# Kernel tuning notes

Measured on AMD Instinct MI355X. Metric: run time of the kernel, lower is better.

The kernel has to match this reference:

```python
import jax, jax.numpy as jnp
import numpy as np

D_MODEL = 2048
NUM_HEADS = 16
D_HEAD = D_MODEL // NUM_HEADS
ROPE_THETA = 10000.0
MAX_SEQ_LEN = 2048
NEG_INF = -1e30


def _rope_tables(seq_len):
    pos = jnp.arange(seq_len, dtype=jnp.float32)[:, None]          # [s,1]
    i = jnp.arange(0, D_HEAD, 2, dtype=jnp.float32)                 # [d/2]
    freqs = 1.0 / (ROPE_THETA ** (i / D_HEAD))
    angles = pos * freqs                                            # [s, d/2]
    return jnp.cos(angles), jnp.sin(angles)


def _apply_rope(x, cos, sin):
    # x: [b,h,s,d]; interleaved pairs: x1 = even dims, x2 = odd dims
    x1 = x[..., 0::2]
    x2 = x[..., 1::2]
    r1 = x1 * cos - x2 * sin
    r2 = x1 * sin + x2 * cos
    return jnp.stack([r1, r2], axis=-1).reshape(x.shape)


def setup_inputs() -> dict:
    key = jax.random.key(0)
    ks = jax.random.split(key, 5)
    b, s = 2, 2048
    scale = 1.0 / np.sqrt(D_MODEL)  # ~kaiming fan_in scale
    return {
        "x": jax.random.normal(ks[0], (b, s, D_MODEL), jnp.float32),
        "Wq": jax.random.normal(ks[1], (D_MODEL, D_MODEL), jnp.float32) * scale,
        "bq": jnp.zeros((D_MODEL,), jnp.float32),
        "Wk": jax.random.normal(ks[2], (D_MODEL, D_MODEL), jnp.float32) * scale,
        "bk": jnp.zeros((D_MODEL,), jnp.float32),
        "Wv": jax.random.normal(ks[3], (D_MODEL, D_MODEL), jnp.float32) * scale,
        "bv": jnp.zeros((D_MODEL,), jnp.float32),
        "Wo": jax.random.normal(ks[4], (D_MODEL, D_MODEL), jnp.float32) * scale,
        "bo": jnp.zeros((D_MODEL,), jnp.float32),
    }


def reference(x, Wq, bq, Wk, bk, Wv, bv, Wo, bo):
    b, s, _ = x.shape
    # QKV projections (torch Linear: y = x @ W.T + b)
    q = x @ Wq.T + bq
    k = x @ Wk.T + bk
    v = x @ Wv.T + bv
    # split heads: b s (h d) -> b h s d
    def split(t):
        return t.reshape(b, s, NUM_HEADS, D_HEAD).transpose(0, 2, 1, 3)
    q, k, v = split(q), split(k), split(v)
    # RoPE
    cos, sin = _rope_tables(s)
    q = _apply_rope(q, cos, sin)
    k = _apply_rope(k, cos, sin)
    # scaled dot-product attention with causal mask
    scores = jnp.einsum('bhqd,bhkd->bhqk', q, k) / jnp.sqrt(jnp.float32(D_HEAD))
    causal = jnp.tril(jnp.ones((s, s), dtype=bool))
    scores = jnp.where(causal[None, None], scores, NEG_INF)
    attn = jax.nn.softmax(scores, axis=-1)
    out = jnp.einsum('bhqk,bhkd->bhqd', attn, v)
    # merge heads and output projection
    out = out.transpose(0, 2, 1, 3).reshape(b, s, D_MODEL)
    return out @ Wo.T + bo
```

## Files before the change

kernel.cpp:

```cpp
#include <hip/hip_runtime.h>
#include <math.h>

#define D_MODEL 2048
#define NH 16
#define DH 128
#define SEQ 2048
#define NBH 32

typedef unsigned short u16;
typedef unsigned int u32;
typedef __attribute__((ext_vector_type(8))) short short8;
typedef __attribute__((ext_vector_type(4))) float floatx4;
typedef __attribute__((ext_vector_type(4))) unsigned short ushort4v;

__device__ __forceinline__ u16 f2bf(float f) {
  u32 u = __builtin_bit_cast(u32, f);
  return (u16)((u + 0x8000u) >> 16);
}
__device__ __forceinline__ float bf2f(u16 h) {
  return __builtin_bit_cast(float, (u32)h << 16);
}

__device__ __forceinline__ void async_load16(const u16* g, u16* l) {
  __builtin_amdgcn_global_load_lds(
      (const __attribute__((address_space(1))) void*)g,
      (__attribute__((address_space(3))) void*)l, 16, 0, 0);
}

template <int CTRL>
__device__ __forceinline__ float dpp_mov(float x) {
  return __builtin_bit_cast(
      float, __builtin_amdgcn_update_dpp(0, __builtin_bit_cast(int, x), CTRL,
                                         0xf, 0xf, false));
}
__device__ __forceinline__ float rmax16(float x) {
  x = fmaxf(x, dpp_mov<0x121>(x));
  x = fmaxf(x, dpp_mov<0x122>(x));
  x = fmaxf(x, dpp_mov<0x124>(x));
  x = fmaxf(x, dpp_mov<0x128>(x));
  return x;
}
__device__ __forceinline__ float radd16(float x) {
  x += dpp_mov<0x121>(x);
  x += dpp_mov<0x122>(x);
  x += dpp_mov<0x124>(x);
  x += dpp_mov<0x128>(x);
  return x;
}

__global__ void cvt_kernel(const float* __restrict__ src, u16* __restrict__ dst,
                           int n) {
  const int i = (blockIdx.x * 256 + threadIdx.x) * 8;
  if (i >= n) return;
  const floatx4 a = *(const floatx4*)(src + i);
  const floatx4 b = *(const floatx4*)(src + i + 4);
  short8 h;
  h[0] = (short)f2bf(a[0]); h[1] = (short)f2bf(a[1]);
  h[2] = (short)f2bf(a[2]); h[3] = (short)f2bf(a[3]);
  h[4] = (short)f2bf(b[0]); h[5] = (short)f2bf(b[1]);
  h[6] = (short)f2bf(b[2]); h[7] = (short)f2bf(b[3]);
  *(short8*)(dst + i) = h;
}

__global__ __launch_bounds__(256, 2) void gemm_async(
    const u16* __restrict__ A, const u16* __restrict__ W0,
    const u16* __restrict__ W1, const u16* __restrict__ W2,
    const float* __restrict__ b0, const float* __restrict__ b1,
    const float* __restrict__ b2, void* __restrict__ C0, void* __restrict__ C1,
    void* __restrict__ C2, const int qkv) {
  __shared__ u16 As[128 * 64];
  __shared__ u16 Bs[128 * 64];
  const int tid = threadIdx.x;
  const int wave = tid >> 6, lane = tid & 63;
  const int lr = lane & 15, lg = lane >> 4;
  const int m0 = blockIdx.y * 128;
  const int wm = (wave & 1) * 64, wn = (wave >> 1) * 64;

  int n0, mode;
  const u16* W;
  const float* bias;
  void* C;
  if (qkv) {
    const int which = blockIdx.x >> 4;
    n0 = (blockIdx.x & 15) * 128;
    W = which == 0 ? W0 : which == 1 ? W1 : W2;
    bias = which == 0 ? b0 : which == 1 ? b1 : b2;
    C = which == 0 ? C0 : which == 1 ? C1 : C2;
    mode = which;
  } else {
    n0 = blockIdx.x * 128;
    W = W0; bias = b0; C = C0; mode = 3;
  }

  floatx4 acc[4][4];
#pragma unroll
  for (int i = 0; i < 4; ++i)
#pragma unroll
    for (int j = 0; j < 4; ++j) {
      floatx4 z = {0.f, 0.f, 0.f, 0.f};
      acc[i][j] = z;
    }

  for (int kt = 0; kt < D_MODEL; kt += 64) {
#pragma unroll
    for (int p = 0; p < 4; ++p) {
      const int s = p * 256 + tid;
      const int row = s >> 3, c = s & 7;
      const int g = c ^ (row & 7);
      async_load16(A + (size_t)(m0 + row) * D_MODEL + kt + g * 8,
                   &As[(p * 256 + wave * 64) * 8]);
    }
#pragma unroll
    for (int p = 0; p < 4; ++p) {
      const int s = p * 256 + tid;
      const int row = s >> 3, c = s & 7;
      const int g = c ^ (row & 7);
      async_load16(W + (size_t)(n0 + row) * D_MODEL + kt + g * 8,
                   &Bs[(p * 256 + wave * 64) * 8]);
    }
    __syncthreads();

#pragma unroll
    for (int ks = 0; ks < 2; ++ks) {
      short8 af[4], bfr[4];
      const int ch = (ks * 4 + lg) ^ (lr & 7);
#pragma unroll
      for (int i = 0; i < 4; ++i)
        af[i] = *(const short8*)&As[(wm + 16 * i + lr) * 64 + ch * 8];
#pragma unroll
      for (int j = 0; j < 4; ++j)
        bfr[j] = *(const short8*)&Bs[(wn + 16 * j + lr) * 64 + ch * 8];
#pragma unroll
      for (int i = 0; i < 4; ++i)
#pragma unroll
        for (int j = 0; j < 4; ++j)
          acc[i][j] = __builtin_amdgcn_mfma_f32_16x16x32_bf16(af[i], bfr[j],
                                                              acc[i][j], 0, 0, 0);
    }
    __syncthreads();
  }

  float bj[4];
  int ncol[4];
#pragma unroll
  for (int j = 0; j < 4; ++j) {
    ncol[j] = n0 + wn + 16 * j + lr;
    bj[j] = bias[ncol[j]];
  }

  if (mode == 3) {
    float* Cf = (float*)C;
#pragma unroll
    for (int i = 0; i < 4; ++i)
#pragma unroll
      for (int r = 0; r < 4; ++r) {
        const int m = m0 + wm + 16 * i + lg * 4 + r;
#pragma unroll
        for (int j = 0; j < 4; ++j)
          Cf[(size_t)m * D_MODEL + ncol[j]] = acc[i][j][r] + bj[j];
      }
  } else if (mode == 2) {
    u16* Ch = (u16*)C;
#pragma unroll
    for (int i = 0; i < 4; ++i)
#pragma unroll
      for (int r = 0; r < 4; ++r) {
        const int m = m0 + wm + 16 * i + lg * 4 + r;
        const int b = m >> 11, s = m & (SEQ - 1);
#pragma unroll
        for (int j = 0; j < 4; ++j) {
          const int h = ncol[j] >> 7, d = ncol[j] & (DH - 1);
          Ch[((size_t)((b * NH + h) * DH + d)) * SEQ + s] =
              f2bf(acc[i][j][r] + bj[j]);
        }
      }
  } else {
    u16* Ch = (u16*)C;
#pragma unroll
    for (int i = 0; i < 4; ++i)
#pragma unroll
      for (int r = 0; r < 4; ++r) {
        const int m = m0 + wm + 16 * i + lg * 4 + r;
        const int b = m >> 11, s = m & (SEQ - 1);
#pragma unroll
        for (int j = 0; j < 4; ++j) {
          const int h = ncol[j] >> 7, d = ncol[j] & (DH - 1);
          Ch[((size_t)((b * NH + h) * SEQ + s)) * DH + d] =
              f2bf(acc[i][j][r] + bj[j]);
        }
      }
  }
}

__global__ void rope_kernel(u16* __restrict__ Q, u16* __restrict__ K) {
  const int idx = blockIdx.x * blockDim.x + threadIdx.x;
  const int p = idx & 63;
  const int s = (idx >> 6) & (SEQ - 1);
  const int bh = idx >> 17;
  if (bh >= NBH) return;
  const float freq = exp2f(-(float)p * (13.287712379549449f / 64.0f));
  const float ang = (float)s * freq;
  float sn, cs;
  sincosf(ang, &sn, &cs);
  const size_t base = ((size_t)bh * SEQ + s) * DH + 2 * p;
  {
    const u32 qq = *(const u32*)(Q + base);
    const float x1 = bf2f((u16)(qq & 0xffffu)), x2 = bf2f((u16)(qq >> 16));
    *(u32*)(Q + base) =
        (u32)f2bf(x1 * cs - x2 * sn) | ((u32)f2bf(x1 * sn + x2 * cs) << 16);
  }
  {
    const u32 kk = *(const u32*)(K + base);
    const float x1 = bf2f((u16)(kk & 0xffffu)), x2 = bf2f((u16)(kk >> 16));
    *(u32*)(K + base) =
        (u32)f2bf(x1 * cs - x2 * sn) | ((u32)f2bf(x1 * sn + x2 * cs) << 16);
  }
}

__global__ __launch_bounds__(256, 2) void attn_kernel(
    const u16* __restrict__ Q, const u16* __restrict__ K,
    const u16* __restrict__ Vt, u16* __restrict__ Oflat) {
  __shared__ u16 Ks[64 * 128];
  __shared__ u16 Vts[128 * 64];
  __shared__ u16 Ps[4 * 32 * 72];
  const int tid = threadIdx.x;
  const int wave = tid >> 6, lane = tid & 63;
  const int lr = lane & 15, lg = lane >> 4;
  const int bh = blockIdx.y;
  const int qt = (blockIdx.y < 16) ? blockIdx.x : (15 - blockIdx.x);
  const size_t qk0 = (size_t)bh * SEQ * DH;
  const int q0 = qt * 128 + wave * 32;
  const float scale = 0.08838834764831845f;
  const float L2E = 1.4426950408889634f;

  short8 qf[2][4];
#pragma unroll
  for (int i = 0; i < 2; ++i)
#pragma unroll
    for (int kb = 0; kb < 4; ++kb)
      qf[i][kb] = *(const short8*)(Q + qk0 + (size_t)(q0 + 16 * i + lr) * DH +
                                   kb * 32 + lg * 8);

  floatx4 o[2][8];
#pragma unroll
  for (int i = 0; i < 2; ++i)
#pragma unroll
    for (int jd = 0; jd < 8; ++jd) {
      floatx4 z = {0.f, 0.f, 0.f, 0.f};
      o[i][jd] = z;
    }
  float mrun[2][4], lrun[2][4];
#pragma unroll
  for (int i = 0; i < 2; ++i)
#pragma unroll
    for (int r = 0; r < 4; ++r) {
      mrun[i][r] = -1e38f;
      lrun[i][r] = 0.f;
    }

  u16* myP = &Ps[wave * 32 * 72];
  const int nkt = 2 * qt + 2;
  for (int kt = 0; kt < nkt; ++kt) {
#pragma unroll
    for (int p = 0; p < 4; ++p) {
      const int s = p * 256 + tid;
      const int row = s >> 4, c = s & 15;
      const int g = c ^ (row & 15);
      async_load16(K + qk0 + (size_t)(kt * 64 + row) * DH + g * 8,
                   &Ks[(p * 256 + wave * 64) * 8]);
    }
#pragma unroll
    for (int p = 0; p < 4; ++p) {
      const int s = p * 256 + tid;
      const int row = s >> 3, c = s & 7;
      const int g = c ^ (row & 7);
      async_load16(Vt + (size_t)bh * DH * SEQ + (size_t)row * SEQ + kt * 64 + g * 8,
                   &Vts[(p * 256 + wave * 64) * 8]);
    }
    __syncthreads();

    floatx4 sacc[2][4];
#pragma unroll
    for (int i = 0; i < 2; ++i)
#pragma unroll
      for (int j = 0; j < 4; ++j) {
        floatx4 z = {0.f, 0.f, 0.f, 0.f};
        sacc[i][j] = z;
      }
#pragma unroll
    for (int kb = 0; kb < 4; ++kb) {
      short8 kf[4];
#pragma unroll
      for (int j = 0; j < 4; ++j)
        kf[j] = *(const short8*)&Ks[(16 * j + lr) * 128 + (((kb * 4 + lg) ^ lr)) * 8];
#pragma unroll
      for (int i = 0; i < 2; ++i)
#pragma unroll
        for (int j = 0; j < 4; ++j)
          sacc[i][j] = __builtin_amdgcn_mfma_f32_16x16x32_bf16(qf[i][kb], kf[j],
                                                               sacc[i][j], 0, 0, 0);
    }

    const bool mask_tile = (kt >= 2 * qt);
#pragma unroll
    for (int i = 0; i < 2; ++i)
#pragma unroll
      for (int j = 0; j < 4; ++j)
#pragma unroll
        for (int r = 0; r < 4; ++r) {
          float v = sacc[i][j][r] * scale;
          if (mask_tile) {
            const int kpos = kt * 64 + 16 * j + lr;
            const int qpos = q0 + 16 * i + lg * 4 + r;
            if (kpos > qpos) v = -1e30f;
          }
          sacc[i][j][r] = v;
        }

    float mnew[2][4], alpha[2][4], rs[2][4];
#pragma unroll
    for (int i = 0; i < 2; ++i)
#pragma unroll
      for (int r = 0; r < 4; ++r) {
        float mx = fmaxf(fmaxf(sacc[i][0][r], sacc[i][1][r]),
                         fmaxf(sacc[i][2][r], sacc[i][3][r]));
        mx = rmax16(mx);
        const float mn = fmaxf(mrun[i][r], mx);
        mnew[i][r] = mn;
        alpha[i][r] = exp2f((mrun[i][r] - mn) * L2E);
        mrun[i][r] = mn;
        rs[i][r] = 0.f;
      }

#pragma unroll
    for (int i = 0; i < 2; ++i)
#pragma unroll
      for (int j = 0; j < 4; ++j)
#pragma unroll
        for (int r = 0; r < 4; ++r) {
          const float pv = exp2f((sacc[i][j][r] - mnew[i][r]) * L2E);
          rs[i][r] += pv;
          myP[(16 * i + lg * 4 + r) * 72 + 16 * j + lr] = f2bf(pv);
        }

#pragma unroll
    for (int i = 0; i < 2; ++i)
#pragma unroll
      for (int r = 0; r < 4; ++r)
        lrun[i][r] = lrun[i][r] * alpha[i][r] + radd16(rs[i][r]);

#pragma unroll
    for (int i = 0; i < 2; ++i)
#pragma unroll
      for (int jd = 0; jd < 8; ++jd)
#pragma unroll
        for (int r = 0; r < 4; ++r) o[i][jd][r] *= alpha[i][r];

    asm volatile("s_waitcnt lgkmcnt(0)" ::: "memory");

#pragma unroll
    for (int kb = 0; kb < 2; ++kb) {
      short8 pf[2];
#pragma unroll
      for (int i = 0; i < 2; ++i)
        pf[i] = *(const short8*)&myP[(16 * i + lr) * 72 + kb * 32 + lg * 8];
#pragma unroll
      for (int jd = 0; jd < 8; ++jd) {
        const short8 vf = *(const short8*)&Vts[(16 * jd + lr) * 64 +
                                               (((kb * 4 + lg) ^ (lr & 7))) * 8];
#pragma unroll
        for (int i = 0; i < 2; ++i)
          o[i][jd] = __builtin_amdgcn_mfma_f32_16x16x32_bf16(pf[i], vf, o[i][jd],
                                                             0, 0, 0);
      }
    }
    __syncthreads();
  }

  const int b = bh >> 4, h = bh & (NH - 1);
#pragma unroll
  for (int i = 0; i < 2; ++i)
#pragma unroll
    for (int r = 0; r < 4; ++r) {
      const int qpos = q0 + 16 * i + lg * 4 + r;
      const float inv = 1.0f / lrun[i][r];
      u16* dst = Oflat + ((size_t)(b * SEQ + qpos)) * D_MODEL + h * DH;
#pragma unroll
      for (int jd = 0; jd < 8; ++jd) dst[16 * jd + lr] = f2bf(o[i][jd][r] * inv);
    }
}

template <int ABF16>
__global__ __launch_bounds__(256, 2) void gemm_kernel(
    const void* __restrict__ Aptr, const float* __restrict__ W,
    const float* __restrict__ bias, void* __restrict__ Cptr, const int mode) {
  __shared__ u16 As[128 * 72];
  __shared__ u16 Bs[128 * 72];
  const int tid = threadIdx.x;
  const int wave = tid >> 6, lane = tid & 63;
  const int lr = lane & 15, lg = lane >> 4;
  const int m0 = blockIdx.y * 128, n0 = blockIdx.x * 128;
  const int wm = (wave & 1) * 64, wn = (wave >> 1) * 64;

  floatx4 acc[4][4];
#pragma unroll
  for (int i = 0; i < 4; ++i)
#pragma unroll
    for (int j = 0; j < 4; ++j) {
      floatx4 z = {0.f, 0.f, 0.f, 0.f};
      acc[i][j] = z;
    }

  for (int kt = 0; kt < D_MODEL; kt += 64) {
    if (ABF16) {
      const u16* A = (const u16*)Aptr;
      const int row0 = tid >> 3, c8 = (tid & 7) * 8;
#pragma unroll
      for (int p = 0; p < 4; ++p) {
        const int row = row0 + p * 32;
        *(short8*)&As[row * 72 + c8] =
            *(const short8*)(A + (size_t)(m0 + row) * D_MODEL + kt + c8);
      }
    } else {
      const float* A = (const float*)Aptr;
      const int row0 = tid >> 4, c4 = (tid & 15) * 4;
#pragma unroll
      for (int p = 0; p < 8; ++p) {
        const int row = row0 + p * 16;
        const floatx4 v =
            *(const floatx4*)(A + (size_t)(m0 + row) * D_MODEL + kt + c4);
        ushort4v h;
        h[0] = f2bf(v[0]); h[1] = f2bf(v[1]); h[2] = f2bf(v[2]); h[3] = f2bf(v[3]);
        *(ushort4v*)&As[row * 72 + c4] = h;
      }
    }
    {
      const int row0 = tid >> 4, c4 = (tid & 15) * 4;
#pragma unroll
      for (int p = 0; p < 8; ++p) {
        const int row = row0 + p * 16;
        const floatx4 v =
            *(const floatx4*)(W + (size_t)(n0 + row) * D_MODEL + kt + c4);
        ushort4v h;
        h[0] = f2bf(v[0]); h[1] = f2bf(v[1]); h[2] = f2bf(v[2]); h[3] = f2bf(v[3]);
        *(ushort4v*)&Bs[row * 72 + c4] = h;
      }
    }
    __syncthreads();
#pragma unroll
    for (int ks = 0; ks < 2; ++ks) {
      short8 af[4], bfr[4];
#pragma unroll
      for (int i = 0; i < 4; ++i)
        af[i] = *(const short8*)&As[(wm + 16 * i + lr) * 72 + ks * 32 + lg * 8];
#pragma unroll
      for (int j = 0; j < 4; ++j)
        bfr[j] = *(const short8*)&Bs[(wn + 16 * j + lr) * 72 + ks * 32 + lg * 8];
#pragma unroll
      for (int i = 0; i < 4; ++i)
#pragma unroll
        for (int j = 0; j < 4; ++j)
          acc[i][j] = __builtin_amdgcn_mfma_f32_16x16x32_bf16(af[i], bfr[j],
                                                              acc[i][j], 0, 0, 0);
    }
    __syncthreads();
  }

  float bj[4];
  int ncol[4];
#pragma unroll
  for (int j = 0; j < 4; ++j) {
    ncol[j] = n0 + wn + 16 * j + lr;
    bj[j] = bias[ncol[j]];
  }

  if (mode == 3) {
    float* C = (float*)Cptr;
#pragma unroll
    for (int i = 0; i < 4; ++i)
#pragma unroll
      for (int r = 0; r < 4; ++r) {
        const int m = m0 + wm + 16 * i + lg * 4 + r;
#pragma unroll
        for (int j = 0; j < 4; ++j)
          C[(size_t)m * D_MODEL + ncol[j]] = acc[i][j][r] + bj[j];
      }
  } else if (mode == 2) {
    u16* C = (u16*)Cptr;
#pragma unroll
    for (int i = 0; i < 4; ++i)
#pragma unroll
      for (int r = 0; r < 4; ++r) {
        const int m = m0 + wm + 16 * i + lg * 4 + r;
        const int b = m >> 11, s = m & (SEQ - 1);
#pragma unroll
        for (int j = 0; j < 4; ++j) {
          const int h = ncol[j] >> 7, d = ncol[j] & (DH - 1);
          C[((size_t)((b * NH + h) * DH + d)) * SEQ + s] = f2bf(acc[i][j][r] + bj[j]);
        }
      }
  } else {
    u16* C = (u16*)Cptr;
#pragma unroll
    for (int i = 0; i < 4; ++i)
#pragma unroll
      for (int r = 0; r < 4; ++r) {
        const int m = m0 + wm + 16 * i + lg * 4 + r;
        const int b = m >> 11, s = m & (SEQ - 1);
#pragma unroll
        for (int j = 0; j < 4; ++j) {
          const int h = ncol[j] >> 7, d = ncol[j] & (DH - 1);
          C[((size_t)((b * NH + h) * SEQ + s)) * DH + d] = f2bf(acc[i][j][r] + bj[j]);
        }
      }
  }
}

extern "C" void kernel_launch(void* const* d_in, const int* in_sizes, int n_in,
                              void* d_out, int out_size, void* d_ws,
                              size_t ws_size, hipStream_t stream) {
  const float* x = (const float*)d_in[0];
  const float* Wq = (const float*)d_in[1];
  const float* bq = (const float*)d_in[2];
  const float* Wk = (const float*)d_in[3];
  const float* bk = (const float*)d_in[4];
  const float* Wv = (const float*)d_in[5];
  const float* bv = (const float*)d_in[6];
  const float* Wo = (const float*)d_in[7];
  const float* bo = (const float*)d_in[8];
  float* out = (float*)d_out;

  const size_t E = (size_t)NBH * SEQ * DH;
  const size_t WE = (size_t)D_MODEL * D_MODEL;
  const size_t need = (4 * E + 3 * WE) * sizeof(u16);

  const dim3 gb(256);

  if (ws_size >= need) {
    u16* xb = (u16*)d_ws;
    u16* wqb = xb + E;
    u16* wkb = wqb + WE;
    u16* wvb = wkb + WE;
    u16* q = wvb + WE;
    u16* k = q + E;
    u16* vt = k + E;
    u16* aflat = xb;
    u16* wob = q;

    cvt_kernel<<<dim3((int)(E / 2048)), gb, 0, stream>>>(x, xb, (int)E);
    cvt_kernel<<<dim3((int)(WE / 2048)), gb, 0, stream>>>(Wq, wqb, (int)WE);
    cvt_kernel<<<dim3((int)(WE / 2048)), gb, 0, stream>>>(Wk, wkb, (int)WE);
    cvt_kernel<<<dim3((int)(WE / 2048)), gb, 0, stream>>>(Wv, wvb, (int)WE);

    gemm_async<<<dim3(48, 32), gb, 0, stream>>>(xb, wqb, wkb, wvb, bq, bk, bv,
                                                q, k, vt, 1);
    rope_kernel<<<dim3((NBH * SEQ * (DH / 2)) / 256), gb, 0, stream>>>(q, k);
    attn_kernel<<<dim3(SEQ / 128, NBH), gb, 0, stream>>>(q, k, vt, aflat);
    cvt_kernel<<<dim3((int)(WE / 2048)), gb, 0, stream>>>(Wo, wob, (int)WE);
    gemm_async<<<dim3(16, 32), gb, 0, stream>>>(aflat, wob, nullptr, nullptr,
                                                bo, nullptr, nullptr, out,
                                                nullptr, nullptr, 0);
  } else {
    u16* q = (u16*)d_ws;
    u16* k = q + E;
    u16* vt = k + E;
    u16* aflat = vt + E;
    const dim3 gg(D_MODEL / 128, (2 * SEQ) / 128);
    gemm_kernel<0><<<gg, gb, 0, stream>>>(x, Wq, bq, q, 0);
    gemm_kernel<0><<<gg, gb, 0, stream>>>(x, Wk, bk, k, 1);
    gemm_kernel<0><<<gg, gb, 0, stream>>>(x, Wv, bv, vt, 2);
    rope_kernel<<<dim3((NBH * SEQ * (DH / 2)) / 256), dim3(256), 0, stream>>>(q, k);
    attn_kernel<<<dim3(SEQ / 128, NBH), gb, 0, stream>>>(q, k, vt, aflat);
    gemm_kernel<1><<<gg, gb, 0, stream>>>(aflat, Wo, bo, out, 3);
  }
}
```

Before: 416.8 us.

## Use 8-wave attention blocks with 16 query rows per wave; merge conversions

The attention kernel now runs 512 threads per block, each wave handling 16 query rows instead of 32. This halves per-wave register state and raises the number of waves sharing each K/V tile in LDS. The softmax scale is folded into the log2e multiply. All five fp32-to-bf16 conversions are merged into one multi-target launch, and Wo gets its own workspace slot so it can be converted up front. The trade-offs are more barrier participants per tile, less Q reuse per K fragment load, and a larger workspace requirement, which could push execution onto the fallback path.

```diff
diff --git a/kernel.cpp b/kernel.cpp
--- a/kernel.cpp
+++ b/kernel.cpp
@@ -48,18 +48,32 @@
   return x;
 }
 
-__global__ void cvt_kernel(const float* __restrict__ src, u16* __restrict__ dst,
-                           int n) {
+__global__ void cvt_multi(const float* __restrict__ s0, u16* __restrict__ d0,
+                          const float* __restrict__ s1, u16* __restrict__ d1,
+                          const float* __restrict__ s2, u16* __restrict__ d2,
+                          const float* __restrict__ s3, u16* __restrict__ d3,
+                          const float* __restrict__ s4, u16* __restrict__ d4,
+                          int nx, int nw) {
+  const float* s;
+  u16* d;
+  int n;
+  switch (blockIdx.y) {
+    case 0: s = s0; d = d0; n = nx; break;
+    case 1: s = s1; d = d1; n = nw; break;
+    case 2: s = s2; d = d2; n = nw; break;
+    case 3: s = s3; d = d3; n = nw; break;
+    default: s = s4; d = d4; n = nw; break;
+  }
   const int i = (blockIdx.x * 256 + threadIdx.x) * 8;
   if (i >= n) return;
-  const floatx4 a = *(const floatx4*)(src + i);
-  const floatx4 b = *(const floatx4*)(src + i + 4);
+  const floatx4 a = *(const floatx4*)(s + i);
+  const floatx4 b = *(const floatx4*)(s + i + 4);
   short8 h;
   h[0] = (short)f2bf(a[0]); h[1] = (short)f2bf(a[1]);
   h[2] = (short)f2bf(a[2]); h[3] = (short)f2bf(a[3]);
   h[4] = (short)f2bf(b[0]); h[5] = (short)f2bf(b[1]);
   h[6] = (short)f2bf(b[2]); h[7] = (short)f2bf(b[3]);
-  *(short8*)(dst + i) = h;
+  *(short8*)(d + i) = h;
 }
 
 __global__ __launch_bounds__(256, 2) void gemm_async(
@@ -217,161 +231,133 @@
   }
 }
 
-__global__ __launch_bounds__(256, 2) void attn_kernel(
+__global__ __launch_bounds__(512, 4) void attn_kernel(
     const u16* __restrict__ Q, const u16* __restrict__ K,
     const u16* __restrict__ Vt, u16* __restrict__ Oflat) {
   __shared__ u16 Ks[64 * 128];
   __shared__ u16 Vts[128 * 64];
-  __shared__ u16 Ps[4 * 32 * 72];
+  __shared__ u16 Ps[8 * 16 * 72];
   const int tid = threadIdx.x;
   const int wave = tid >> 6, lane = tid & 63;
   const int lr = lane & 15, lg = lane >> 4;
   const int bh = blockIdx.y;
   const int qt = (blockIdx.y < 16) ? blockIdx.x : (15 - blockIdx.x);
   const size_t qk0 = (size_t)bh * SEQ * DH;
-  const int q0 = qt * 128 + wave * 32;
-  const float scale = 0.08838834764831845f;
-  const float L2E = 1.4426950408889634f;
-
-  short8 qf[2][4];
-#pragma unroll
-  for (int i = 0; i < 2; ++i)
-#pragma unroll
-    for (int kb = 0; kb < 4; ++kb)
-      qf[i][kb] = *(const short8*)(Q + qk0 + (size_t)(q0 + 16 * i + lr) * DH +
-                                   kb * 32 + lg * 8);
-
-  floatx4 o[2][8];
-#pragma unroll
-  for (int i = 0; i < 2; ++i)
-#pragma unroll
-    for (int jd = 0; jd < 8; ++jd) {
-      floatx4 z = {0.f, 0.f, 0.f, 0.f};
-      o[i][jd] = z;
-    }
-  float mrun[2][4], lrun[2][4];
-#pragma unroll
-  for (int i = 0; i < 2; ++i)
-#pragma unroll
-    for (int r = 0; r < 4; ++r) {
-      mrun[i][r] = -1e38f;
-      lrun[i][r] = 0.f;
-    }
-
-  u16* myP = &Ps[wave * 32 * 72];
+  const int q0 = qt * 128 + wave * 16;
+  const float SL2E = 0.08838834764831845f * 1.4426950408889634f;
+
+  short8 qf[4];
+#pragma unroll
+  for (int kb = 0; kb < 4; ++kb)
+    qf[kb] = *(const short8*)(Q + qk0 + (size_t)(q0 + lr) * DH + kb * 32 + lg * 8);
+
+  floatx4 o[8];
+#pragma unroll
+  for (int jd = 0; jd < 8; ++jd) {
+    floatx4 z = {0.f, 0.f, 0.f, 0.f};
+    o[jd] = z;
+  }
+  float mrun[4], lrun[4];
+#pragma unroll
+  for (int r = 0; r < 4; ++r) {
+    mrun[r] = -1e38f;
+    lrun[r] = 0.f;
+  }
+
+  u16* myP = &Ps[wave * 16 * 72];
   const int nkt = 2 * qt + 2;
   for (int kt = 0; kt < nkt; ++kt) {
 #pragma unroll
-    for (int p = 0; p < 4; ++p) {
-      const int s = p * 256 + tid;
+    for (int p = 0; p < 2; ++p) {
+      const int s = p * 512 + tid;
       const int row = s >> 4, c = s & 15;
       const int g = c ^ (row & 15);
       async_load16(K + qk0 + (size_t)(kt * 64 + row) * DH + g * 8,
-                   &Ks[(p * 256 + wave * 64) * 8]);
-    }
-#pragma unroll
-    for (int p = 0; p < 4; ++p) {
-      const int s = p * 256 + tid;
+                   &Ks[(p * 512 + wave * 64) * 8]);
+    }
+#pragma unroll
+    for (int p = 0; p < 2; ++p) {
+      const int s = p * 512 + tid;
       const int row = s >> 3, c = s & 7;
       const int g = c ^ (row & 7);
       async_load16(Vt + (size_t)bh * DH * SEQ + (size_t)row * SEQ + kt * 64 + g * 8,
-                   &Vts[(p * 256 + wave * 64) * 8]);
+                   &Vts[(p * 512 + wave * 64) * 8]);
     }
     __syncthreads();
 
-    floatx4 sacc[2][4];
-#pragma unroll
-    for (int i = 0; i < 2; ++i)
-#pragma unroll
-      for (int j = 0; j < 4; ++j) {
-        floatx4 z = {0.f, 0.f, 0.f, 0.f};
-        sacc[i][j] = z;
-      }
+    floatx4 sacc[4];
+#pragma unroll
+    for (int j = 0; j < 4; ++j) {
+      floatx4 z = {0.f, 0.f, 0.f, 0.f};
+      sacc[j] = z;
+    }
 #pragma unroll
     for (int kb = 0; kb < 4; ++kb) {
       short8 kf[4];
 #pragma unroll
       for (int j = 0; j < 4; ++j)
-        kf[j] = *(const short8*)&Ks[(16 * j + lr) * 128 + (((kb * 4 + lg) ^ lr)) * 8];
-#pragma unroll
-      for (int i = 0; i < 2; ++i)
-#pragma unroll
-        for (int j = 0; j < 4; ++j)
-          sacc[i][j] = __builtin_amdgcn_mfma_f32_16x16x32_bf16(qf[i][kb], kf[j],
-                                                               sacc[i][j], 0, 0, 0);
+        kf[j] = *(const short8*)&Ks[(16 * j + lr) * 128 + ((kb * 4 + lg) ^ lr) * 8];
+#pragma unroll
+      for (int j = 0; j < 4; ++j)
+        sacc[j] = __builtin_amdgcn_mfma_f32_16x16x32_bf16(qf[kb], kf[j],
+                                                          sacc[j], 0, 0, 0);
     }
 
     const bool mask_tile = (kt >= 2 * qt);
 #pragma unroll
-    for (int i = 0; i < 2; ++i)
-#pragma unroll
-      for (int j = 0; j < 4; ++j)
-#pragma unroll
-        for (int r = 0; r < 4; ++r) {
-          float v = sacc[i][j][r] * scale;
-          if (mask_tile) {
-            const int kpos = kt * 64 + 16 * j + lr;
-            const int qpos = q0 + 16 * i + lg * 4 + r;
-            if (kpos > qpos) v = -1e30f;
-          }
-          sacc[i][j][r] = v;
+    for (int j = 0; j < 4; ++j)
+#pragma unroll
+      for (int r = 0; r < 4; ++r) {
+        float v = sacc[j][r] * SL2E;
+        if (mask_tile) {
+          const int kpos = kt * 64 + 16 * j + lr;
+          const int qpos = q0 + lg * 4 + r;
+          if (kpos > qpos) v = -1e30f;
         }
-
-    float mnew[2][4], alpha[2][4], rs[2][4];
-#pragma unroll
-    for (int i = 0; i < 2; ++i)
-#pragma unroll
-      for (int r = 0; r < 4; ++r) {
-        float mx = fmaxf(fmaxf(sacc[i][0][r], sacc[i][1][r]),
-                         fmaxf(sacc[i][2][r], sacc[i][3][r]));
-        mx = rmax16(mx);
-        const float mn = fmaxf(mrun[i][r], mx);
-        mnew[i][r] = mn;
-        alpha[i][r] = exp2f((mrun[i][r] - mn) * L2E);
-        mrun[i][r] = mn;
-        rs[i][r] = 0.f;
-      }
-
-#pragma unroll
-    for (int i = 0; i < 2; ++i)
-#pragma unroll
-      for (int j = 0; j < 4; ++j)
-#pragma unroll
-        for (int r = 0; r < 4; ++r) {
-          const float pv = exp2f((sacc[i][j][r] - mnew[i][r]) * L2E);
-          rs[i][r] += pv;
-          myP[(16 * i + lg * 4 + r) * 72 + 16 * j + lr] = f2bf(pv);
-        }
-
-#pragma unroll
-    for (int i = 0; i < 2; ++i)
-#pragma unroll
-      for (int r = 0; r < 4; ++r)
-        lrun[i][r] = lrun[i][r] * alpha[i][r] + radd16(rs[i][r]);
-
-#pragma unroll
-    for (int i = 0; i < 2; ++i)
-#pragma unroll
-      for (int jd = 0; jd < 8; ++jd)
-#pragma unroll
-        for (int r = 0; r < 4; ++r) o[i][jd][r] *= alpha[i][r];
+        sacc[j][r] = v;
+      }
+
+    float mnew[4], alpha[4], rs[4];
+#pragma unroll
+    for (int r = 0; r < 4; ++r) {
+      float mx = fmaxf(fmaxf(sacc[0][r], sacc[1][r]),
+                       fmaxf(sacc[2][r], sacc[3][r]));
+      mx = rmax16(mx);
+      const float mn = fmaxf(mrun[r], mx);
+      mnew[r] = mn;
+      alpha[r] = exp2f(mrun[r] - mn);
+      mrun[r] = mn;
+      rs[r] = 0.f;
+    }
+
+#pragma unroll
+    for (int j = 0; j < 4; ++j)
+#pragma unroll
+      for (int r = 0; r < 4; ++r) {
+        const float pv = exp2f(sacc[j][r] - mnew[r]);
+        rs[r] += pv;
+        myP[(lg * 4 + r) * 72 + 16 * j + lr] = f2bf(pv);
+      }
+
+#pragma unroll
+    for (int r = 0; r < 4; ++r)
+      lrun[r] = lrun[r] * alpha[r] + radd16(rs[r]);
+
+#pragma unroll
+    for (int jd = 0; jd < 8; ++jd)
+#pragma unroll
+      for (int r = 0; r < 4; ++r) o[jd][r] *= alpha[r];
 
     asm volatile("s_waitcnt lgkmcnt(0)" ::: "memory");
 
 #pragma unroll
     for (int kb = 0; kb < 2; ++kb) {
-      short8 pf[2];
-#pragma unroll
-      for (int i = 0; i < 2; ++i)
-        pf[i] = *(const short8*)&myP[(16 * i + lr) * 72 + kb * 32 + lg * 8];
+      const short8 pf = *(const short8*)&myP[lr * 72 + kb * 32 + lg * 8];
 #pragma unroll
       for (int jd = 0; jd < 8; ++jd) {
         const short8 vf = *(const short8*)&Vts[(16 * jd + lr) * 64 +
-                                               (((kb * 4 + lg) ^ (lr & 7))) * 8];
-#pragma unroll
-        for (int i = 0; i < 2; ++i)
-          o[i][jd] = __builtin_amdgcn_mfma_f32_16x16x32_bf16(pf[i], vf, o[i][jd],
-                                                             0, 0, 0);
+                                               ((kb * 4 + lg) ^ (lr & 7)) * 8];
+        o[jd] = __builtin_amdgcn_mfma_f32_16x16x32_bf16(pf, vf, o[jd], 0, 0, 0);
       }
     }
     __syncthreads();
@@ -379,15 +365,13 @@
 
   const int b = bh >> 4, h = bh & (NH - 1);
 #pragma unroll
-  for (int i = 0; i < 2; ++i)
-#pragma unroll
-    for (int r = 0; r < 4; ++r) {
-      const int qpos = q0 + 16 * i + lg * 4 + r;
-      const float inv = 1.0f / lrun[i][r];
-      u16* dst = Oflat + ((size_t)(b * SEQ + qpos)) * D_MODEL + h * DH;
-#pragma unroll
-      for (int jd = 0; jd < 8; ++jd) dst[16 * jd + lr] = f2bf(o[i][jd][r] * inv);
-    }
+  for (int r = 0; r < 4; ++r) {
+    const int qpos = q0 + lg * 4 + r;
+    const float inv = 1.0f / lrun[r];
+    u16* dst = Oflat + ((size_t)(b * SEQ + qpos)) * D_MODEL + h * DH;
+#pragma unroll
+    for (int jd = 0; jd < 8; ++jd) dst[16 * jd + lr] = f2bf(o[jd][r] * inv);
+  }
 }
 
 template <int ABF16>
@@ -532,7 +516,7 @@
 
   const size_t E = (size_t)NBH * SEQ * DH;
   const size_t WE = (size_t)D_MODEL * D_MODEL;
-  const size_t need = (4 * E + 3 * WE) * sizeof(u16);
+  const size_t need = (4 * E + 4 * WE) * sizeof(u16);
 
   const dim3 gb(256);
 
@@ -541,22 +525,19 @@
     u16* wqb = xb + E;
     u16* wkb = wqb + WE;
     u16* wvb = wkb + WE;
-    u16* q = wvb + WE;
+    u16* wob = wvb + WE;
+    u16* q = wob + WE;
     u16* k = q + E;
     u16* vt = k + E;
     u16* aflat = xb;
-    u16* wob = q;
-
-    cvt_kernel<<<dim3((int)(E / 2048)), gb, 0, stream>>>(x, xb, (int)E);
-    cvt_kernel<<<dim3((int)(WE / 2048)), gb, 0, stream>>>(Wq, wqb, (int)WE);
-    cvt_kernel<<<dim3((int)(WE / 2048)), gb, 0, stream>>>(Wk, wkb, (int)WE);
-    cvt_kernel<<<dim3((int)(WE / 2048)), gb, 0, stream>>>(Wv, wvb, (int)WE);
+
+    cvt_multi<<<dim3((int)(E / 2048), 5), gb, 0, stream>>>(
+        x, xb, Wq, wqb, Wk, wkb, Wv, wvb, Wo, wob, (int)E, (int)WE);
 
     gemm_async<<<dim3(48, 32), gb, 0, stream>>>(xb, wqb, wkb, wvb, bq, bk, bv,
                                                 q, k, vt, 1);
     rope_kernel<<<dim3((NBH * SEQ * (DH / 2)) / 256), gb, 0, stream>>>(q, k);
-    attn_kernel<<<dim3(SEQ / 128, NBH), gb, 0, stream>>>(q, k, vt, aflat);
-    cvt_kernel<<<dim3((int)(WE / 2048)), gb, 0, stream>>>(Wo, wob, (int)WE);
+    attn_kernel<<<dim3(SEQ / 128, NBH), dim3(512), 0, stream>>>(q, k, vt, aflat);
     gemm_async<<<dim3(16, 32), gb, 0, stream>>>(aflat, wob, nullptr, nullptr,
                                                 bo, nullptr, nullptr, out,
                                                 nullptr, nullptr, 0);
@@ -570,7 +551,7 @@
     gemm_kernel<0><<<gg, gb, 0, stream>>>(x, Wk, bk, k, 1);
     gemm_kernel<0><<<gg, gb, 0, stream>>>(x, Wv, bv, vt, 2);
     rope_kernel<<<dim3((NBH * SEQ * (DH / 2)) / 256), dim3(256), 0, stream>>>(q, k);
-    attn_kernel<<<dim3(SEQ / 128, NBH), gb, 0, stream>>>(q, k, vt, aflat);
+    attn_kernel<<<dim3(SEQ / 128, NBH), dim3(512), 0, stream>>>(q, k, vt, aflat);
     gemm_kernel<1><<<gg, gb, 0, stream>>>(aflat, Wo, bo, out, 3);
   }
 }
```

Result: no change. 417.2 us (+0.1%).
